# Kernel tuning notes

Hardware: AMD Instinct MI355X
Metric: run time of the kernel (lower is better)

## Reference

```python
import jax, jax.numpy as jnp
import numpy as np

B, C, T, H, W = 1, 512, 4, 32, 32
NUM_HEADS = 8
HEAD_DIM = C // NUM_HEADS


def setup_inputs() -> dict:
    key = jax.random.key(0)
    k1, k2, k3 = jax.random.split(key, 3)
    x = jax.random.normal(k1, (B, C, T, H, W), dtype=jnp.float32)
    w_qkv = jax.random.normal(k2, (3 * C, C), dtype=jnp.float32) * (1.0 / np.sqrt(C))
    w_out = jax.random.normal(k3, (C, C), dtype=jnp.float32) * (1.0 / np.sqrt(C))
    b_out = jnp.zeros((C,), dtype=jnp.float32)
    return {"x": x, "w_qkv": w_qkv, "w_out": w_out, "b_out": b_out}


def reference(x, w_qkv, w_out, b_out):
    b, c, t, h, w = x.shape
    n = t * h * w
    nh, hd = NUM_HEADS, c // NUM_HEADS
    x_flat = x.reshape(b, c, n)                      # [B,C,N]
    # 1x1 Conv3d == pointwise channel GEMM
    qkv = jnp.einsum('oc,bcn->bon', w_qkv, x_flat)   # [B,3C,N]
    q, k, v = jnp.split(qkv, 3, axis=1)
    q = q.reshape(b, nh, hd, n)
    k = k.reshape(b, nh, hd, n)
    v = v.reshape(b, nh, hd, n)
    dots = jnp.einsum('bhdi,bhdj->bhij', q, k) * (hd ** -0.5)  # [B,h,N,N]
    attn = jax.nn.softmax(dots, axis=-1)
    out = jnp.einsum('bhij,bhdj->bhdi', attn, v)     # [B,h,d,N]
    out = out.reshape(b, c, n)
    out = jnp.einsum('oc,bcn->bon', w_out, out) + b_out[None, :, None]
    return out.reshape(b, c, t, h, w) + x
```

## Files before the change

### kernel.cpp

```cpp
#include <hip/hip_runtime.h>
#include <hip/hip_bf16.h>


#define N_TOK 4096
#define C_DIM 512
#define NH    8
#define HD    64

#define QSCALE  0.18033688011112042f

typedef __bf16 bf16x8 __attribute__((ext_vector_type(8)));
typedef float f32x4 __attribute__((ext_vector_type(4)));

__device__ __forceinline__ f32x4 mfma16(bf16x8 a, bf16x8 b, f32x4 c) {
    return __builtin_amdgcn_mfma_f32_16x16x32_bf16(a, b, c, 0, 0, 0);
}

__device__ __forceinline__ bool probe_f32(const unsigned short* x) {
    int lane = threadIdx.x & 63;
    int hits = 0;
    #pragma unroll
    for (int r = 0; r < 4; r++) {
        unsigned short u = x[(lane * 4 + r) * 2];
        hits += (((u >> 7) & 0xFF) >= 140) ? 1 : 0;
    }
    #pragma unroll
    for (int off = 1; off < 64; off <<= 1) hits += __shfl_xor(hits, off);
    return hits >= 8;
}

__global__ __launch_bounds__(256) void prepare(
    const void* __restrict__ xv, const void* __restrict__ wq,
    const void* __restrict__ wo, const void* __restrict__ bo,
    __hip_bfloat16* __restrict__ xt, __hip_bfloat16* __restrict__ wqc,
    __hip_bfloat16* __restrict__ woc, __hip_bfloat16* __restrict__ bc)
{
    bool f32 = probe_f32((const unsigned short*)xv);
    int b = blockIdx.x, tid = threadIdx.x;
    if (b < 512) {
        __shared__ __hip_bfloat16 t[64][68];
        int n0 = (b & 63) * 64, c0 = (b >> 6) * 64;
        int nl = tid & 15, cl = tid >> 4;
        #pragma unroll
        for (int p = 0; p < 4; p++) {
            int c = cl + p * 16;
            ushort4 pk;
            if (f32) {
                float4 v = *reinterpret_cast<const float4*>(
                    (const float*)xv + (size_t)(c0 + c) * N_TOK + n0 + nl * 4);
                union { unsigned short u; __hip_bfloat16 h; } a0, a1, a2, a3;
                a0.h = __float2bfloat16(v.x); a1.h = __float2bfloat16(v.y);
                a2.h = __float2bfloat16(v.z); a3.h = __float2bfloat16(v.w);
                pk.x = a0.u; pk.y = a1.u; pk.z = a2.u; pk.w = a3.u;
            } else {
                pk = *reinterpret_cast<const ushort4*>(
                    (const __hip_bfloat16*)xv + (size_t)(c0 + c) * N_TOK + n0 + nl * 4);
            }
            *reinterpret_cast<ushort4*>(&t[c][nl * 4]) = pk;
        }
        __syncthreads();
        int cc = tid & 15, nr = tid >> 4;
        #pragma unroll
        for (int p = 0; p < 4; p++) {
            int n = nr + p * 16;
            ushort4 v;
            v.x = *reinterpret_cast<unsigned short*>(&t[cc * 4 + 0][n]);
            v.y = *reinterpret_cast<unsigned short*>(&t[cc * 4 + 1][n]);
            v.z = *reinterpret_cast<unsigned short*>(&t[cc * 4 + 2][n]);
            v.w = *reinterpret_cast<unsigned short*>(&t[cc * 4 + 3][n]);
            *reinterpret_cast<ushort4*>(xt + (size_t)(n0 + n) * C_DIM + c0 + cc * 4) = v;
        }
    } else {
        const int N1 = 3 * C_DIM * C_DIM, N2 = C_DIM * C_DIM, N3 = C_DIM;
        int total4 = (N1 + N2 + N3) >> 2;
        int stride = 128 * 256;
        for (int g = (b - 512) * 256 + tid; g < total4; g += stride) {
            int i = g * 4;
            const void* src; __hip_bfloat16* dst; int j;
            if (i < N1)           { src = wq; dst = wqc; j = i; }
            else if (i < N1 + N2) { src = wo; dst = woc; j = i - N1; }
            else                  { src = bo; dst = bc;  j = i - N1 - N2; }
            ushort4 pk;
            if (f32) {
                float4 v = *reinterpret_cast<const float4*>((const float*)src + j);
                union { unsigned short u; __hip_bfloat16 h; } a0, a1, a2, a3;
                a0.h = __float2bfloat16(v.x); a1.h = __float2bfloat16(v.y);
                a2.h = __float2bfloat16(v.z); a3.h = __float2bfloat16(v.w);
                pk.x = a0.u; pk.y = a1.u; pk.z = a2.u; pk.w = a3.u;
            } else {
                pk = *reinterpret_cast<const ushort4*>((const __hip_bfloat16*)src + j);
            }
            *reinterpret_cast<ushort4*>(dst + j) = pk;
        }
    }
}

__global__ __launch_bounds__(128) void qkv_gemm(
    const __hip_bfloat16* __restrict__ w,
    const __hip_bfloat16* __restrict__ xt,
    __hip_bfloat16* __restrict__ qt,
    unsigned char* __restrict__ kvg)
{
    __shared__ alignas(16) unsigned char stg[2][8192];
    int tid = threadIdx.x, lane = tid & 63, wv = tid >> 6;
    int l15 = lane & 15, quad = lane >> 4;
    int n0w = blockIdx.x * 128 + wv * 64;
    int m0w = blockIdx.y * 64;
    f32x4 acc[4][4] = {};
    bf16x8 a[4][4], b[4][4];
    #pragma unroll
    for (int pl = 0; pl < 3; pl++) {
        int kn = pl * 32 + quad * 8;
        #pragma unroll
        for (int i = 0; i < 4; i++)
            a[pl][i] = *reinterpret_cast<const bf16x8*>(xt + (n0w + i * 16 + l15) * 512 + kn);
        #pragma unroll
        for (int j = 0; j < 4; j++)
            b[pl][j] = *reinterpret_cast<const bf16x8*>(w + (m0w + j * 16 + l15) * 512 + kn);
    }
    #pragma unroll
    for (int kk = 0; kk < 16; kk++) {
        int cur = kk & 3;
        if (kk + 3 < 16) {
            int nxt = (kk + 3) & 3;
            int kn = (kk + 3) * 32 + quad * 8;
            #pragma unroll
            for (int i = 0; i < 4; i++)
                a[nxt][i] = *reinterpret_cast<const bf16x8*>(xt + (n0w + i * 16 + l15) * 512 + kn);
            #pragma unroll
            for (int j = 0; j < 4; j++)
                b[nxt][j] = *reinterpret_cast<const bf16x8*>(w + (m0w + j * 16 + l15) * 512 + kn);
        }
        #pragma unroll
        for (int i = 0; i < 4; i++)
            #pragma unroll
            for (int j = 0; j < 4; j++)
                acc[i][j] = mfma16(a[cur][i], b[cur][j], acc[i][j]);
    }
    int kind = m0w >> 9;
    int h = (m0w >> 6) & 7;
    int jb = n0w >> 6;
    unsigned char* sb = &stg[wv][0];
    #pragma unroll
    for (int i = 0; i < 4; i++)
        #pragma unroll
        for (int j = 0; j < 4; j++)
            #pragma unroll
            for (int r = 0; r < 4; r++) {
                int nn = i * 16 + quad * 4 + r;
                int dd = j * 16 + l15;
                float v = acc[i][j][r];
                int row, cg, byo;
                if (kind == 0)      { row = nn; cg = dd >> 3;              byo = (dd & 7) * 2; v *= QSCALE; }
                else if (kind == 1) { row = nn; cg = (dd >> 3) ^ (nn & 7); byo = (dd & 7) * 2; }
                else {
                    row = dd;
                    int cc = ((nn >> 5) << 2) | ((nn >> 2) & 3);
                    cg = cc ^ (dd & 7);
                    byo = ((nn >> 4) & 1) * 8 + (nn & 3) * 2;
                }
                int phys = cg ^ ((row >> 1) & 7);
                *reinterpret_cast<__hip_bfloat16*>(sb + row * 128 + phys * 16 + byo)
                    = __float2bfloat16(v);
            }
    unsigned char* gbase;
    if (kind == 0) gbase = (unsigned char*)(qt + ((size_t)h * N_TOK + n0w) * HD);
    else           gbase = kvg + (((size_t)h * 64 + jb) << 14) + (kind == 2 ? 8192 : 0);
    #pragma unroll
    for (int it = 0; it < 8; it++) {
        int idx = it * 64 + lane;
        int row = idx >> 3, phys = (idx & 7) ^ ((idx >> 4) & 7);
        uint4 val = *reinterpret_cast<const uint4*>(sb + row * 128 + phys * 16);
        *reinterpret_cast<uint4*>(gbase + idx * 16) = val;
    }
}

__global__ __launch_bounds__(256) void attn_kernel(
    const __hip_bfloat16* __restrict__ qt,
    const unsigned char* __restrict__ kv,
    __hip_bfloat16* __restrict__ Opart,
    float* __restrict__ lpart,
    __hip_bfloat16* __restrict__ ot,
    int tbase, int trem)
{
    __shared__ alignas(16) unsigned char kvb[4][16384];
    int tid = threadIdx.x, lane = tid & 63, wv = tid >> 6;
    int l15 = lane & 15, quad = lane >> 4;
    int s7 = l15 & 7;
    int h = blockIdx.x >> 4;
    int i0 = (blockIdx.x & 15) * 256 + wv * 64;
    int kslice = blockIdx.y;
    const unsigned char* kvh = kv + ((size_t)h << 20);

    int jt0 = kslice * tbase + min(kslice, trem);
    int ntile = tbase + (kslice < trem ? 1 : 0);

    bf16x8 qB[4][2];
    #pragma unroll
    for (int g = 0; g < 4; g++)
        #pragma unroll
        for (int hf = 0; hf < 2; hf++)
            qB[g][hf] = *reinterpret_cast<const bf16x8*>(
                qt + (h * N_TOK + i0 + g * 16 + l15) * HD + hf * 32 + quad * 8);

    bf16x8 vones;
    #pragma unroll
    for (int i = 0; i < 8; i++) vones[i] = (__bf16)1.0f;

    f32x4 oacc[4][4] = {};
    f32x4 lsum[4] = {};

    int koff[2], vo[2];
    #pragma unroll
    for (int hf = 0; hf < 2; hf++)
        koff[hf] = l15 * 128 + (((hf * 4 + quad) ^ s7) << 4);
    #pragma unroll
    for (int p = 0; p < 2; p++)
        vo[p] = l15 * 128 + (((p * 4 + quad) ^ s7) << 4);

    auto stage = [&](int jb, int buf) {
        const unsigned char* s = kvh + ((size_t)jb << 14) + wv * 4096 + lane * 16;
        unsigned char* d = &kvb[buf][0] + wv * 4096;
        #pragma unroll
        for (int it = 0; it < 4; it++)
            __builtin_amdgcn_global_load_lds(
                (const __attribute__((address_space(1))) void*)(s + it * 1024),
                (__attribute__((address_space(3))) void*)(d + it * 1024),
                16, 0, 0);
    };

    auto body = [&](const unsigned char* kb) {
        const unsigned char* vb = kb + 8192;
        bf16x8 kf[8];
        #pragma unroll
        for (int nt = 0; nt < 4; nt++)
            #pragma unroll
            for (int hf = 0; hf < 2; hf++)
                kf[nt * 2 + hf] = *reinterpret_cast<const bf16x8*>(kb + nt * 2048 + koff[hf]);
        bf16x8 vf[4][2];
        #pragma unroll
        for (int db = 0; db < 4; db++)
            #pragma unroll
            for (int p = 0; p < 2; p++)
                vf[db][p] = *reinterpret_cast<const bf16x8*>(vb + db * 2048 + vo[p]);

        f32x4 sA[4], sB[4];
        #pragma unroll
        for (int nt = 0; nt < 4; nt++) {
            f32x4 z = {};
            z = mfma16(kf[nt * 2], qB[0][0], z);
            sA[nt] = mfma16(kf[nt * 2 + 1], qB[0][1], z);
        }
        #pragma unroll
        for (int g = 0; g < 4; g++) {
            f32x4* scur = (g & 1) ? sB : sA;
            f32x4* snxt = (g & 1) ? sA : sB;
            if (g < 3) {
                #pragma unroll
                for (int nt = 0; nt < 4; nt++) {
                    f32x4 z = {};
                    z = mfma16(kf[nt * 2], qB[g + 1][0], z);
                    snxt[nt] = mfma16(kf[nt * 2 + 1], qB[g + 1][1], z);
                }
            }
            bf16x8 pf[2];
            #pragma unroll
            for (int p = 0; p < 2; p++)
                #pragma unroll
                for (int i = 0; i < 4; i++) {
                    pf[p][i]     = (__bf16)__builtin_amdgcn_exp2f(scur[p * 2][i]);
                    pf[p][i + 4] = (__bf16)__builtin_amdgcn_exp2f(scur[p * 2 + 1][i]);
                }
            #pragma unroll
            for (int p = 0; p < 2; p++) {
                #pragma unroll
                for (int db = 0; db < 4; db++)
                    oacc[g][db] = mfma16(pf[p], vf[db][p], oacc[g][db]);
                lsum[g] = mfma16(pf[p], vones, lsum[g]);
            }
        }
    };

    stage(jt0, 0);
    if (ntile > 1) stage(jt0 + 1, 1);
    if (ntile > 2) stage(jt0 + 2, 2);
    for (int t = 0; t < ntile; t++) {
        if (t + 2 < ntile)      asm volatile("s_waitcnt vmcnt(8)" ::: "memory");
        else if (t + 1 < ntile) asm volatile("s_waitcnt vmcnt(4)" ::: "memory");
        else                    asm volatile("s_waitcnt vmcnt(0)" ::: "memory");
        __builtin_amdgcn_s_barrier();
        __builtin_amdgcn_sched_barrier(0);
        if (t + 3 < ntile) stage(jt0 + t + 3, (t + 3) & 3);
        body(&kvb[t & 3][0]);
    }

    if (Opart) {
        __hip_bfloat16* Ob = Opart + (size_t)kslice * (NH * N_TOK * HD);
        float* lb = lpart + (size_t)kslice * (NH * N_TOK);
        #pragma unroll
        for (int g = 0; g < 4; g++) {
            #pragma unroll
            for (int db = 0; db < 4; db++)
                #pragma unroll
                for (int r = 0; r < 4; r++) {
                    int i = i0 + g * 16 + quad * 4 + r;
                    Ob[(h * N_TOK + i) * HD + db * 16 + l15] =
                        __float2bfloat16(oacc[g][db][r]);
                }
            if (l15 == 0)
                #pragma unroll
                for (int r = 0; r < 4; r++)
                    lb[h * N_TOK + i0 + g * 16 + quad * 4 + r] = lsum[g][r];
        }
    } else {
        #pragma unroll
        for (int g = 0; g < 4; g++)
            #pragma unroll
            for (int db = 0; db < 4; db++)
                #pragma unroll
                for (int r = 0; r < 4; r++) {
                    int i = i0 + g * 16 + quad * 4 + r;
                    ot[i * C_DIM + h * HD + db * 16 + l15] =
                        __float2bfloat16(oacc[g][db][r] / lsum[g][r]);
                }
    }
}

__global__ __launch_bounds__(256) void combine_kernel(
    const __hip_bfloat16* __restrict__ Opart, const float* __restrict__ lpart,
    __hip_bfloat16* __restrict__ ot, int splitk)
{
    int tid = blockIdx.x * 256 + threadIdx.x;
    int h = tid >> 16, rem = tid & 65535;
    int q = rem >> 4, d4 = rem & 15;
    size_t off = ((size_t)(h * N_TOK + q) * HD) + d4 * 4;
    float o[4] = {};
    float l = 0.f;
    for (int k = 0; k < splitk; k++) {
        ushort4 u = *reinterpret_cast<const ushort4*>(
            Opart + (size_t)k * (NH * N_TOK * HD) + off);
        union { unsigned short us; __hip_bfloat16 h; } c0, c1, c2, c3;
        c0.us = u.x; c1.us = u.y; c2.us = u.z; c3.us = u.w;
        o[0] += __bfloat162float(c0.h); o[1] += __bfloat162float(c1.h);
        o[2] += __bfloat162float(c2.h); o[3] += __bfloat162float(c3.h);
        l += lpart[k * (NH * N_TOK) + h * N_TOK + q];
    }
    float inv = 1.0f / l;
    union { unsigned long long u; __hip_bfloat16 b[4]; } pk;
    #pragma unroll
    for (int i = 0; i < 4; i++) pk.b[i] = __float2bfloat16(o[i] * inv);
    *reinterpret_cast<unsigned long long*>(ot + q * C_DIM + h * HD + d4 * 4) = pk.u;
}

__global__ __launch_bounds__(256) void proj_gemm(
    const __hip_bfloat16* __restrict__ w,
    const __hip_bfloat16* __restrict__ ot,
    const __hip_bfloat16* __restrict__ bias,
    const void* __restrict__ xv,
    void* __restrict__ outv)
{
    bool f32 = probe_f32((const unsigned short*)xv);
    int tid = threadIdx.x, lane = tid & 63, wv = tid >> 6;
    int l15 = lane & 15, quad = lane >> 4;
    int m0 = blockIdx.y * 32;
    int n0 = blockIdx.x * 128 + wv * 32;
    f32x4 acc[2][2] = {};
    bf16x8 a[4][2], b[4][2];
    #pragma unroll
    for (int pl = 0; pl < 3; pl++) {
        int kn = pl * 32 + quad * 8;
        #pragma unroll
        for (int mt = 0; mt < 2; mt++)
            a[pl][mt] = *reinterpret_cast<const bf16x8*>(w + (m0 + mt * 16 + l15) * 512 + kn);
        #pragma unroll
        for (int nt = 0; nt < 2; nt++)
            b[pl][nt] = *reinterpret_cast<const bf16x8*>(ot + (n0 + nt * 16 + l15) * 512 + kn);
    }
    #pragma unroll
    for (int kk = 0; kk < 16; kk++) {
        int cur = kk & 3;
        if (kk + 3 < 16) {
            int nxt = (kk + 3) & 3;
            int kn = (kk + 3) * 32 + quad * 8;
            #pragma unroll
            for (int mt = 0; mt < 2; mt++)
                a[nxt][mt] = *reinterpret_cast<const bf16x8*>(w + (m0 + mt * 16 + l15) * 512 + kn);
            #pragma unroll
            for (int nt = 0; nt < 2; nt++)
                b[nxt][nt] = *reinterpret_cast<const bf16x8*>(ot + (n0 + nt * 16 + l15) * 512 + kn);
        }
        #pragma unroll
        for (int mt = 0; mt < 2; mt++)
            #pragma unroll
            for (int nt = 0; nt < 2; nt++)
                acc[mt][nt] = mfma16(a[cur][mt], b[cur][nt], acc[mt][nt]);
    }
    #pragma unroll
    for (int mt = 0; mt < 2; mt++)
        #pragma unroll
        for (int nt = 0; nt < 2; nt++)
            #pragma unroll
            for (int r = 0; r < 4; r++) {
                int m = m0 + mt * 16 + quad * 4 + r;
                int n = n0 + nt * 16 + l15;
                int idx = m * N_TOK + n;
                float xr = f32 ? ((const float*)xv)[idx]
                               : __bfloat162float(((const __hip_bfloat16*)xv)[idx]);
                float v = acc[mt][nt][r] + __bfloat162float(bias[m]) + xr;
                if (f32) ((float*)outv)[idx] = v;
                else     ((__hip_bfloat16*)outv)[idx] = __float2bfloat16(v);
            }
}

extern "C" void kernel_launch(void* const* d_in, const int* in_sizes, int n_in,
                              void* d_out, int out_size, void* d_ws, size_t ws_size,
                              hipStream_t stream) {
    const void* x     = d_in[0];
    const void* w_qkv = d_in[1];
    const void* w_out = d_in[2];
    const void* b_out = d_in[3];

    char* ws = (char*)d_ws;
    const size_t MB = 1024 * 1024;
    __hip_bfloat16* xt  = (__hip_bfloat16*)(ws);
    __hip_bfloat16* ot  = (__hip_bfloat16*)(ws);
    __hip_bfloat16* qt  = (__hip_bfloat16*)(ws + 4 * MB);
    unsigned char*  kv  = (unsigned char*) (ws + 8 * MB);
    __hip_bfloat16* wqc = (__hip_bfloat16*)(ws + 16 * MB);
    __hip_bfloat16* woc = (__hip_bfloat16*)(ws + 16 * MB + 0x180000);
    __hip_bfloat16* bc  = (__hip_bfloat16*)(ws + 16 * MB + 0x200000);

    const size_t pbase   = 16 * MB + 0x200800;
    const size_t o_slice = (size_t)NH * N_TOK * HD * 2;
    const size_t l_slice = (size_t)NH * N_TOK * 4;
    int nslice = 1;
    if      (ws_size >= pbase + 4 * (o_slice + l_slice)) nslice = 4;
    else if (ws_size >= pbase + 3 * (o_slice + l_slice)) nslice = 3;
    else if (ws_size >= pbase + 2 * (o_slice + l_slice)) nslice = 2;
    __hip_bfloat16* Opart = (nslice > 1) ? (__hip_bfloat16*)(ws + pbase) : nullptr;
    float* lpart = (nslice > 1) ? (float*)(ws + pbase + (size_t)nslice * o_slice) : nullptr;

    prepare<<<640, 256, 0, stream>>>(x, w_qkv, w_out, b_out, xt, wqc, woc, bc);
    qkv_gemm<<<dim3(32, 24), 128, 0, stream>>>(wqc, xt, qt, kv);

    int tbase = 64 / nslice, trem = 64 % nslice;
    attn_kernel<<<dim3(128, nslice), 256, 0, stream>>>(
        qt, kv, Opart, lpart, ot, tbase, trem);
    if (nslice > 1)
        combine_kernel<<<2048, 256, 0, stream>>>(Opart, lpart, ot, nslice);

    proj_gemm<<<dim3(32, 16), 256, 0, stream>>>(woc, ot, bc, x, d_out);
}
```

Measured before the change: 160.2 us.

## Stage QKV GEMM operands through swizzled LDS with async global-to-LDS loads

The QKV projection GEMM used to load its A and B fragments from global memory straight into registers with a 4-deep register pipeline. It now copies 64-wide K chunks of x and w into double-buffered, XOR-swizzled shared memory using global_load_lds, with explicit vmcnt waits and barriers. The wave tiles then read their fragments from LDS. The aim is to get coalesced global reads, share the weight tile between the two waves, and overlap the next chunk's load with the current MFMAs. The cost is more LDS use and barrier synchronisation per chunk, and the staging buffer for the epilogue now reuses the sx region.

```diff
diff --git a/kernel.cpp b/kernel.cpp
--- a/kernel.cpp
+++ b/kernel.cpp
@@ -101,46 +101,85 @@
     __hip_bfloat16* __restrict__ qt,
     unsigned char* __restrict__ kvg)
 {
-    __shared__ alignas(16) unsigned char stg[2][8192];
+    __shared__ alignas(16) unsigned char sx[2][16384];
+    __shared__ alignas(16) unsigned char swt[2][8192];
     int tid = threadIdx.x, lane = tid & 63, wv = tid >> 6;
     int l15 = lane & 15, quad = lane >> 4;
-    int n0w = blockIdx.x * 128 + wv * 64;
+    int n0b = blockIdx.x * 128;
+    int n0w = n0b + wv * 64;
     int m0w = blockIdx.y * 64;
+    int rl = lane >> 3, cs = lane & 7;
+
     f32x4 acc[4][4] = {};
-    bf16x8 a[4][4], b[4][4];
-    #pragma unroll
-    for (int pl = 0; pl < 3; pl++) {
-        int kn = pl * 32 + quad * 8;
-        #pragma unroll
-        for (int i = 0; i < 4; i++)
-            a[pl][i] = *reinterpret_cast<const bf16x8*>(xt + (n0w + i * 16 + l15) * 512 + kn);
-        #pragma unroll
-        for (int j = 0; j < 4; j++)
-            b[pl][j] = *reinterpret_cast<const bf16x8*>(w + (m0w + j * 16 + l15) * 512 + kn);
-    }
-    #pragma unroll
-    for (int kk = 0; kk < 16; kk++) {
-        int cur = kk & 3;
-        if (kk + 3 < 16) {
-            int nxt = (kk + 3) & 3;
-            int kn = (kk + 3) * 32 + quad * 8;
+
+    auto stageF = [&](int c, int buf) {
+        #pragma unroll
+        for (int k = 0; k < 8; k++) {
+            int g = wv * 8 + k;
+            int row = g * 8 + rl;
+            const unsigned char* src = (const unsigned char*)xt
+                + (size_t)(n0b + row) * 1024 + c * 128 + ((cs ^ (row & 7)) << 4);
+            __builtin_amdgcn_global_load_lds(
+                (const __attribute__((address_space(1))) void*)src,
+                (__attribute__((address_space(3))) void*)(&sx[buf][g * 1024]),
+                16, 0, 0);
+        }
+        #pragma unroll
+        for (int k = 0; k < 4; k++) {
+            int g = wv * 4 + k;
+            int row = g * 8 + rl;
+            const unsigned char* src = (const unsigned char*)w
+                + (size_t)(m0w + row) * 1024 + c * 128 + ((cs ^ (row & 7)) << 4);
+            __builtin_amdgcn_global_load_lds(
+                (const __attribute__((address_space(1))) void*)src,
+                (__attribute__((address_space(3))) void*)(&swt[buf][g * 1024]),
+                16, 0, 0);
+        }
+    };
+
+    auto compute = [&](int buf) {
+        bf16x8 af[2][4], bfr[2][4];
+        #pragma unroll
+        for (int hf = 0; hf < 2; hf++) {
+            #pragma unroll
+            for (int i = 0; i < 4; i++) {
+                int row = wv * 64 + i * 16 + l15;
+                af[hf][i] = *reinterpret_cast<const bf16x8*>(
+                    &sx[buf][row * 128 + (((hf * 4 + quad) ^ (row & 7)) << 4)]);
+            }
+            #pragma unroll
+            for (int j = 0; j < 4; j++) {
+                int row = j * 16 + l15;
+                bfr[hf][j] = *reinterpret_cast<const bf16x8*>(
+                    &swt[buf][row * 128 + (((hf * 4 + quad) ^ (row & 7)) << 4)]);
+            }
+        }
+        #pragma unroll
+        for (int hf = 0; hf < 2; hf++)
             #pragma unroll
             for (int i = 0; i < 4; i++)
-                a[nxt][i] = *reinterpret_cast<const bf16x8*>(xt + (n0w + i * 16 + l15) * 512 + kn);
-            #pragma unroll
-            for (int j = 0; j < 4; j++)
-                b[nxt][j] = *reinterpret_cast<const bf16x8*>(w + (m0w + j * 16 + l15) * 512 + kn);
-        }
-        #pragma unroll
-        for (int i = 0; i < 4; i++)
-            #pragma unroll
-            for (int j = 0; j < 4; j++)
-                acc[i][j] = mfma16(a[cur][i], b[cur][j], acc[i][j]);
-    }
+                #pragma unroll
+                for (int j = 0; j < 4; j++)
+                    acc[i][j] = mfma16(af[hf][i], bfr[hf][j], acc[i][j]);
+    };
+
+    stageF(0, 0);
+    #pragma unroll
+    for (int c = 0; c < 8; c++) {
+        if (c + 1 < 8) stageF(c + 1, (c + 1) & 1);
+        if (c + 1 < 8) asm volatile("s_waitcnt vmcnt(12)" ::: "memory");
+        else           asm volatile("s_waitcnt vmcnt(0)" ::: "memory");
+        __builtin_amdgcn_s_barrier();
+        __builtin_amdgcn_sched_barrier(0);
+        compute(c & 1);
+        asm volatile("" ::: "memory");
+        __builtin_amdgcn_s_barrier();
+    }
+
     int kind = m0w >> 9;
     int h = (m0w >> 6) & 7;
     int jb = n0w >> 6;
-    unsigned char* sb = &stg[wv][0];
+    unsigned char* sb = &sx[0][wv * 8192];
     #pragma unroll
     for (int i = 0; i < 4; i++)
         #pragma unroll
```

Result: faster. 146.9 us (-8.3%).
